# Performance work log

Hardware: AMD Instinct MI355X
Metric: run time of the kernel (lower is better)

## Reference

```python
import jax, jax.numpy as jnp
import numpy as np

L, S, M, N, E, H = 1024, 1024, 256, 8, 512, 8


def embed_rotary(x, cos, sin):
    # x: [B, T, E]; interleaved rotate-half as in RotaryPositionEncoding.embed_rotary
    x2 = jnp.stack([-x[..., 1::2], x[..., 0::2]], axis=-1).reshape(x.shape)
    return x * cos + x2 * sin


def setup_inputs() -> dict:
    key = jax.random.key(0)
    ks = jax.random.split(key, 12)
    return {
        "query": jax.random.normal(ks[0], (L, N, E), jnp.float32),
        "key": jax.random.normal(ks[1], (S, N, E), jnp.float32),
        "value": jax.random.normal(ks[2], (S, N, E), jnp.float32),
        "in_proj_weight": jax.random.normal(ks[3], (3 * E, E), jnp.float32) / np.sqrt(E).astype(np.float32),
        "in_proj_bias": jnp.zeros((3 * E,), jnp.float32),
        "out_proj_weight": jax.random.normal(ks[4], (E, E), jnp.float32) / np.sqrt(E).astype(np.float32),
        "out_proj_bias": jnp.zeros((E,), jnp.float32),
        "rot_q": jax.random.normal(ks[5], (N, L, E, 2), jnp.float32),
        "rot_k": jax.random.normal(ks[6], (N, S, E, 2), jnp.float32),
        "k_mem": jax.random.normal(ks[7], (M, N, E), jnp.float32),
        "v_mem": jax.random.normal(ks[8], (M, N, E), jnp.float32),
        "gate_attn": jax.random.normal(ks[9], (H,), jnp.float32),
        "mem_mask": jax.random.randint(ks[10], (N, M), 0, 2).astype(bool),
        "num_heads": H,
    }


def reference(query, key, value, in_proj_weight, in_proj_bias, out_proj_weight,
              out_proj_bias, rot_q, rot_k, k_mem, v_mem, gate_attn, mem_mask, num_heads):
    L_, N_, E_ = query.shape
    S_ = key.shape[0]
    H_ = num_heads
    hd = E_ // H_
    scale = float(hd) ** -0.5
    # separate q/k/v projections (qkv not identical path)
    q = query @ in_proj_weight[:E_].T + in_proj_bias[:E_]
    k = key @ in_proj_weight[E_:2 * E_].T + in_proj_bias[E_:2 * E_]
    v = value @ in_proj_weight[2 * E_:].T + in_proj_bias[2 * E_:]
    q = q * scale
    # inline rotary PE (applied in batch-first layout, then back)
    q = embed_rotary(q.transpose(1, 0, 2), rot_q[..., 0], rot_q[..., 1]).transpose(1, 0, 2)
    k = embed_rotary(k.transpose(1, 0, 2), rot_k[..., 0], rot_k[..., 1]).transpose(1, 0, 2)
    qh = q.reshape(L_, N_, H_, hd).transpose(1, 2, 0, 3)  # [N,H,L,hd]
    kh = k.reshape(S_, N_, H_, hd).transpose(1, 2, 0, 3)  # [N,H,S,hd]
    vh = v.reshape(S_, N_, H_, hd).transpose(1, 2, 0, 3)
    scores = jnp.einsum('nhld,nhsd->nhls', qh, kh)
    # slot-competition: softmax over queries (slots), then renormalize over keys
    w = jax.nn.softmax(scores, axis=2) + 1e-8
    w = w / w.sum(axis=-1, keepdims=True)
    attn = jnp.einsum('nhls,nhsd->nhld', w, vh)
    # memorizing-transformer style memory K/V branch with sigmoid head gating
    Mm = k_mem.shape[0]
    km = k_mem.reshape(Mm, N_, H_, hd).transpose(1, 2, 0, 3)  # [N,H,M,hd]
    vm = v_mem.reshape(Mm, N_, H_, hd).transpose(1, 2, 0, 3)
    sm = jnp.einsum('nhld,nhmd->nhlm', qh, km)
    sm = jnp.where(mem_mask[:, None, None, :], -1e9, sm)  # additive -inf mask
    wm = jax.nn.softmax(sm, axis=-1)
    om = jnp.einsum('nhlm,nhmd->nhld', wm, vm)
    gate = jax.nn.sigmoid(gate_attn)[None, :, None, None]  # [1,H,1,1]
    attn = gate * om + (1.0 - gate) * attn
    out = attn.transpose(2, 0, 1, 3).reshape(L_, N_, E_)  # back to [L,N,E]
    return out @ out_proj_weight.T + out_proj_bias
```

## Files before the change

### kernel.cpp

```cpp
#include <hip/hip_runtime.h>
#include <hip/hip_bf16.h>

typedef __hip_bfloat16 bf16;
typedef __bf16 bf16x8 __attribute__((ext_vector_type(8)));
typedef float f32x4 __attribute__((ext_vector_type(4)));

#define LQ 1024
#define SK 1024
#define MMEM 256
#define NB 8
#define EE 512
#define NH 8
#define HD 64
#define NBH 64

__device__ inline __bf16 tobf(float f) {
  __hip_bfloat16 h = __float2bfloat16(f);
  return *reinterpret_cast<__bf16*>(&h);
}
__device__ inline float bf2f(__bf16 x) {
  unsigned short u; __builtin_memcpy(&u, &x, 2);
  unsigned int v = (unsigned int)u << 16;
  float f; __builtin_memcpy(&f, &v, 4);
  return f;
}
__device__ inline f32x4 MFMA(bf16x8 a, bf16x8 b, f32x4 c) {
  return __builtin_amdgcn_mfma_f32_16x16x32_bf16(a, b, c, 0, 0, 0);
}

__device__ inline void gload_lds16(const bf16* g, void* l) {
  __builtin_amdgcn_global_load_lds(
      (const __attribute__((address_space(1))) void*)g,
      (__attribute__((address_space(3))) void*)l, 16, 0, 0);
}

__device__ inline bf16x8 load8(const float* p) {
  float4 a = *(const float4*)p;
  float4 b = *(const float4*)(p + 4);
  bf16x8 r;
  r[0] = tobf(a.x); r[1] = tobf(a.y); r[2] = tobf(a.z); r[3] = tobf(a.w);
  r[4] = tobf(b.x); r[5] = tobf(b.y); r[6] = tobf(b.z); r[7] = tobf(b.w);
  return r;
}

#define CVT_T0 524288
#define CVT_T3 98304
#define CVT_T4 32768
__global__ __launch_bounds__(256) void convert5(
    const float* __restrict__ q, const float* __restrict__ k,
    const float* __restrict__ v, const float* __restrict__ w,
    const float* __restrict__ o, bf16* __restrict__ qc, bf16* __restrict__ kc,
    bf16* __restrict__ vc, bf16* __restrict__ wc, bf16* __restrict__ oc)
{
  long long t = (long long)blockIdx.x * 256 + threadIdx.x;
  const float* src; bf16* dst; long long idx;
  if (t < CVT_T0)               { src = q; dst = qc; idx = t; }
  else if (t < 2 * CVT_T0)      { src = k; dst = kc; idx = t - CVT_T0; }
  else if (t < 3 * CVT_T0)      { src = v; dst = vc; idx = t - 2 * CVT_T0; }
  else if (t < 3 * CVT_T0 + CVT_T3) { src = w; dst = wc; idx = t - 3 * CVT_T0; }
  else                          { src = o; dst = oc; idx = t - 3 * CVT_T0 - CVT_T3; }
  *(bf16x8*)(dst + idx * 8) = load8(src + idx * 8);
}

__global__ __launch_bounds__(256) void gemm_proj3(
    const bf16* __restrict__ qc, const bf16* __restrict__ kc,
    const bf16* __restrict__ vc, const bf16* __restrict__ ipwb,
    const float* __restrict__ ipb, bf16* __restrict__ pq,
    bf16* __restrict__ pk, bf16* __restrict__ v_raw)
{
  __shared__ __align__(16) char smem[33792];
  __bf16* As = (__bf16*)smem;
  __bf16* Bs = (__bf16*)(smem + 16384);
  const int z = blockIdx.z;
  const bf16* A = (z == 0) ? qc : (z == 1) ? kc : vc;
  const bf16* W = ipwb + (long long)z * EE * EE;
  const float* bias = ipb + z * EE;
  const float alpha = (z == 0) ? 0.125f : 1.f;
  const int tm0 = blockIdx.y << 7, tn0 = blockIdx.x << 7;
  const int t = threadIdx.x;
  const int wave = t >> 6, lane = t & 63;
  const int wrow0 = (wave & 1) << 6, wcol0 = (wave >> 1) << 6;
  const int m16 = lane & 15, quad = lane >> 4;

  const f32x4 zero = {0.f, 0.f, 0.f, 0.f};
  f32x4 acc[4][4];
#pragma unroll
  for (int mi = 0; mi < 4; ++mi)
#pragma unroll
    for (int ni = 0; ni < 4; ++ni) acc[mi][ni] = zero;

  const bf16* Ab = A + (long long)tm0 * EE;
  const bf16* Bb = W + (long long)tn0 * EE;
  const int ob_u = wave << 10;

  for (int k0 = 0; k0 < EE; k0 += 64) {
#pragma unroll
    for (int c = 0; c < 4; ++c) {
      int ob = (c << 12) + ob_u;
      int obl = ob + (lane << 4);
      int row = obl >> 7;
      int ce = (obl & 127) >> 1;
      gload_lds16(Ab + (long long)row * EE + k0 + ce, smem + ob);
      gload_lds16(Bb + (long long)row * EE + k0 + ce, smem + 16384 + ob);
    }
    __syncthreads();
#pragma unroll
    for (int kh = 0; kh < 2; ++kh) {
      bf16x8 av[4], bv[4];
#pragma unroll
      for (int i = 0; i < 4; ++i) {
        av[i] = *(bf16x8*)(As + ((wrow0 + (i << 4) + m16) << 6) + (kh << 5) + (quad << 3));
        bv[i] = *(bf16x8*)(Bs + ((wcol0 + (i << 4) + m16) << 6) + (kh << 5) + (quad << 3));
      }
#pragma unroll
      for (int mi = 0; mi < 4; ++mi)
#pragma unroll
        for (int ni = 0; ni < 4; ++ni)
          acc[mi][ni] = MFMA(av[mi], bv[ni], acc[mi][ni]);
    }
    __syncthreads();
  }

  __bf16 (*Cs)[132] = (__bf16(*)[132])smem;
#pragma unroll
  for (int mi = 0; mi < 4; ++mi)
#pragma unroll
    for (int ni = 0; ni < 4; ++ni) {
      int col = wcol0 + (ni << 4) + m16;
      float bv = bias[tn0 + col];
#pragma unroll
      for (int r = 0; r < 4; ++r)
        Cs[wrow0 + (mi << 4) + (quad << 2) + r][col] =
            tobf((acc[mi][ni][r] + bv) * alpha);
    }
  __syncthreads();
  bf16* O = (z == 0) ? pq : (z == 1) ? pk : v_raw;
  const int crow = t >> 1, ch0 = (t & 1) << 6;
  long long gb = (long long)(tm0 + crow) * EE + tn0 + ch0;
#pragma unroll
  for (int j = 0; j < 64; j += 8)
    *(uint4*)(O + gb + j) = *(uint4*)&Cs[crow][ch0 + j];
}

__global__ __launch_bounds__(256) void rotary_kernel(
    const bf16* __restrict__ pq, const bf16* __restrict__ pk,
    const float* __restrict__ rot_q, const float* __restrict__ rot_k,
    bf16* __restrict__ Qh, bf16* __restrict__ Kh)
{
  const bf16* src = blockIdx.y ? pk : pq;
  const float* rot = blockIdx.y ? rot_k : rot_q;
  bf16* dst = blockIdx.y ? Kh : Qh;
  const int t = threadIdx.x;
  const int row = (blockIdx.x << 2) + (t >> 6);
  const int e0 = (t & 63) << 3;
  const int l = row >> 3, n = row & 7;
  bf16x8 x = *(const bf16x8*)(src + (long long)row * EE + e0);
  const float* rp = rot + ((((long long)n * LQ + l) * EE + e0) << 1);
  __bf16 vals[8];
#pragma unroll
  for (int j = 0; j < 8; j += 2) {
    float4 cs4 = *(const float4*)(rp + (j << 1));
    float x0 = bf2f(x[j]);
    float x1 = bf2f(x[j + 1]);
    vals[j]     = tobf(x0 * cs4.x - x1 * cs4.y);
    vals[j + 1] = tobf(x1 * cs4.z + x0 * cs4.w);
  }
  const int h = e0 >> 6, d0 = e0 & 63;
  *(uint4*)(dst + (((long long)(n * NH + h) * LQ + l) * HD + d0)) = *(uint4*)vals;
}

__global__ __launch_bounds__(256) void colsum_kernel(
    const bf16* __restrict__ Qh, const bf16* __restrict__ Kh,
    float* __restrict__ csum)
{
  __shared__ __align__(16) __bf16 Ks[64][72];
  __shared__ __align__(16) __bf16 Qs[64][72];
  __shared__ float cpart[64][2];
  const int b = blockIdx.y;
  const int st0 = blockIdx.x << 6;
  const int t = threadIdx.x;
  const int lrow = t >> 2, lcol = (t & 3) << 4;
  const int wave = t >> 6, lane = t & 63;
  const int wm = (wave & 1) << 5, wn = (wave >> 1) << 5;
  const int m16 = lane & 15, quad = lane >> 4;

  {
    const bf16* kp = Kh + ((long long)b * SK + st0 + lrow) * HD + lcol;
    *(bf16x8*)&Ks[lrow][lcol] = *(const bf16x8*)kp;
    *(bf16x8*)&Ks[lrow][lcol + 8] = *(const bf16x8*)(kp + 8);
  }
  __syncthreads();
  bf16x8 bk[2][2];
#pragma unroll
  for (int ni = 0; ni < 2; ++ni)
#pragma unroll
    for (int kh = 0; kh < 2; ++kh)
      bk[ni][kh] = *(bf16x8*)&Ks[wn + (ni << 4) + m16][(kh << 5) + (quad << 3)];
  __syncthreads();

  const f32x4 zero = {0.f, 0.f, 0.f, 0.f};
  float colp[2] = {0.f, 0.f};
  for (int lt = 0; lt < 16; ++lt) {
    const bf16* qp = Qh + ((long long)b * LQ + (lt << 6) + lrow) * HD + lcol;
    *(bf16x8*)&Qs[lrow][lcol] = *(const bf16x8*)qp;
    *(bf16x8*)&Qs[lrow][lcol + 8] = *(const bf16x8*)(qp + 8);
    __syncthreads();
    f32x4 s00 = zero, s01 = zero, s10 = zero, s11 = zero;
#pragma unroll
    for (int kh = 0; kh < 2; ++kh) {
      bf16x8 a0 = *(bf16x8*)&Qs[wm + m16][(kh << 5) + (quad << 3)];
      bf16x8 a1 = *(bf16x8*)&Qs[wm + 16 + m16][(kh << 5) + (quad << 3)];
      s00 = MFMA(a0, bk[0][kh], s00);
      s01 = MFMA(a0, bk[1][kh], s01);
      s10 = MFMA(a1, bk[0][kh], s10);
      s11 = MFMA(a1, bk[1][kh], s11);
    }
    f32x4 sacc[2][2] = {{s00, s01}, {s10, s11}};
#pragma unroll
    for (int mi = 0; mi < 2; ++mi)
#pragma unroll
      for (int ni = 0; ni < 2; ++ni)
#pragma unroll
        for (int r = 0; r < 4; ++r)
          colp[ni] += __expf(sacc[mi][ni][r]);
    __syncthreads();
  }
  for (int ni = 0; ni < 2; ++ni) {
    float v = colp[ni];
    v += __shfl_down(v, 32, 64);
    v += __shfl_down(v, 16, 64);
    if (quad == 0) cpart[wn + (ni << 4) + m16][wm >> 5] = v;
  }
  __syncthreads();
  if (t < 64) csum[b * SK + st0 + t] = cpart[t][0] + cpart[t][1];
}

__global__ __launch_bounds__(256) void vsum_kernel(
    const bf16* __restrict__ Vt, float* __restrict__ Vsum)
{
  int wid = blockIdx.x * 4 + (threadIdx.x >> 6);
  int lane = threadIdx.x & 63;
  const bf16* p = Vt + (long long)wid * SK + lane * 16;
  float s = 0.f;
  bf16x8 v0 = *(const bf16x8*)p;
  bf16x8 v1 = *(const bf16x8*)(p + 8);
#pragma unroll
  for (int j = 0; j < 8; ++j) s += bf2f(v0[j]) + bf2f(v1[j]);
  for (int off = 32; off; off >>= 1) s += __shfl_down(s, off, 64);
  if (lane == 0) Vsum[wid] = s;
}

__global__ __launch_bounds__(256) void attn_flash(
    const bf16* __restrict__ Qh, const bf16* __restrict__ Kh,
    const bf16* __restrict__ Vt, const float* __restrict__ csum,
    const float* __restrict__ Vsum, bf16* __restrict__ attn)
{
  __shared__ __align__(16) __bf16 Ks[64][72];
  __shared__ __align__(16) __bf16 Vs[64][72];
  __shared__ __align__(16) __bf16 Ps[64][72];
  __shared__ float rcs[SK];
  __shared__ float rpart[64][2];
  const int b = blockIdx.y;
  const int tm0 = blockIdx.x << 6;
  const int t = threadIdx.x;
  const int lrow = t >> 2, lcol = (t & 3) << 4;
  const int wave = t >> 6, lane = t & 63;
  const int wm = (wave & 1) << 5, wn = (wave >> 1) << 5;
  const int m16 = lane & 15, quad = lane >> 4;

#pragma unroll
  for (int i = 0; i < 4; ++i)
    rcs[t + i * 256] = 1.f / csum[b * SK + t + i * 256];
  {
    const bf16* qp = Qh + ((long long)b * LQ + tm0 + lrow) * HD + lcol;
    *(bf16x8*)&Ks[lrow][lcol] = *(const bf16x8*)qp;
    *(bf16x8*)&Ks[lrow][lcol + 8] = *(const bf16x8*)(qp + 8);
  }
  __syncthreads();
  bf16x8 aq[2][2];
#pragma unroll
  for (int mi = 0; mi < 2; ++mi)
#pragma unroll
    for (int kh = 0; kh < 2; ++kh)
      aq[mi][kh] = *(bf16x8*)&Ks[wm + (mi << 4) + m16][(kh << 5) + (quad << 3)];
  __syncthreads();

  const f32x4 zero = {0.f, 0.f, 0.f, 0.f};
  f32x4 o00 = zero, o01 = zero, o10 = zero, o11 = zero;
  float rsumr[2][4] = {{0.f, 0.f, 0.f, 0.f}, {0.f, 0.f, 0.f, 0.f}};

  for (int st = 0; st < 16; ++st) {
    const bf16* kp = Kh + ((long long)b * SK + (st << 6) + lrow) * HD + lcol;
    *(bf16x8*)&Ks[lrow][lcol] = *(const bf16x8*)kp;
    *(bf16x8*)&Ks[lrow][lcol + 8] = *(const bf16x8*)(kp + 8);
    const bf16* vp = Vt + ((long long)b * HD + lrow) * SK + (st << 6) + lcol;
    *(bf16x8*)&Vs[lrow][lcol] = *(const bf16x8*)vp;
    *(bf16x8*)&Vs[lrow][lcol + 8] = *(const bf16x8*)(vp + 8);
    __syncthreads();
    f32x4 s00 = zero, s01 = zero, s10 = zero, s11 = zero;
#pragma unroll
    for (int kh = 0; kh < 2; ++kh) {
      bf16x8 b0 = *(bf16x8*)&Ks[wn + m16][(kh << 5) + (quad << 3)];
      bf16x8 b1 = *(bf16x8*)&Ks[wn + 16 + m16][(kh << 5) + (quad << 3)];
      s00 = MFMA(aq[0][kh], b0, s00);
      s01 = MFMA(aq[0][kh], b1, s01);
      s10 = MFMA(aq[1][kh], b0, s10);
      s11 = MFMA(aq[1][kh], b1, s11);
    }
    f32x4 sacc[2][2] = {{s00, s01}, {s10, s11}};
#pragma unroll
    for (int mi = 0; mi < 2; ++mi)
#pragma unroll
      for (int ni = 0; ni < 2; ++ni) {
        int col = wn + (ni << 4) + m16;
        float rc = rcs[(st << 6) + col];
#pragma unroll
        for (int r = 0; r < 4; ++r) {
          float p = __expf(sacc[mi][ni][r]) * rc;
          rsumr[mi][r] += p;
          Ps[wm + (mi << 4) + (quad << 2) + r][col] = tobf(p);
        }
      }
    __syncthreads();
#pragma unroll
    for (int kh = 0; kh < 2; ++kh) {
      bf16x8 ap0 = *(bf16x8*)&Ps[wm + m16][(kh << 5) + (quad << 3)];
      bf16x8 ap1 = *(bf16x8*)&Ps[wm + 16 + m16][(kh << 5) + (quad << 3)];
      bf16x8 bv0 = *(bf16x8*)&Vs[wn + m16][(kh << 5) + (quad << 3)];
      bf16x8 bv1 = *(bf16x8*)&Vs[wn + 16 + m16][(kh << 5) + (quad << 3)];
      o00 = MFMA(ap0, bv0, o00);
      o01 = MFMA(ap0, bv1, o01);
      o10 = MFMA(ap1, bv0, o10);
      o11 = MFMA(ap1, bv1, o11);
    }
    __syncthreads();
  }
#pragma unroll
  for (int mi = 0; mi < 2; ++mi)
#pragma unroll
    for (int r = 0; r < 4; ++r) {
      float v = rsumr[mi][r];
      v += __shfl_xor(v, 1, 64);
      v += __shfl_xor(v, 2, 64);
      v += __shfl_xor(v, 4, 64);
      v += __shfl_xor(v, 8, 64);
      if (m16 == 0) rpart[wm + (mi << 4) + (quad << 2) + r][wn >> 5] = v;
    }
  __syncthreads();
  const float* vs = Vsum + b * HD;
  f32x4 oacc[2][2] = {{o00, o01}, {o10, o11}};
  for (int mi = 0; mi < 2; ++mi)
    for (int ni = 0; ni < 2; ++ni) {
      int col = wn + (ni << 4) + m16;
      float vsc = 1e-8f * vs[col];
      for (int r = 0; r < 4; ++r) {
        int row = wm + (mi << 4) + (quad << 2) + r;
        float rs = rpart[row][0] + rpart[row][1];
        Ps[row][col] = tobf((oacc[mi][ni][r] + vsc) / (rs + (float)SK * 1e-8f));
      }
    }
  __syncthreads();
  uint4 u0 = *(uint4*)&Ps[lrow][lcol];
  uint4 u1 = *(uint4*)&Ps[lrow][lcol + 8];
  long long gb = ((long long)b * LQ + tm0 + lrow) * HD + lcol;
  *(uint4*)(attn + gb) = u0;
  *(uint4*)(attn + gb + 8) = u1;
}

__global__ __launch_bounds__(256) void mem_flash(
    const bf16* __restrict__ Qh, const bf16* __restrict__ km,
    const bf16* __restrict__ vmt, const int* __restrict__ mask,
    bf16* __restrict__ omb)
{
  __shared__ __align__(16) __bf16 Ks[64][72];
  __shared__ __align__(16) __bf16 Vs[64][72];
  __shared__ __align__(16) __bf16 Ps[64][72];
  __shared__ float mskf[MMEM];
  __shared__ float rpart[64][2];
  const int b = blockIdx.y;
  const int n = b >> 3;
  const int tm0 = blockIdx.x << 6;
  const int t = threadIdx.x;
  const int wave = t >> 6, lane = t & 63;
  const int wm = (wave & 1) << 5, wn = (wave >> 1) << 5;
  const int m16 = lane & 15, quad = lane >> 4;
  const int lrow = t >> 2, lcol = (t & 3) << 4;

  mskf[t] = mask[n * MMEM + t] ? 0.f : 1.f;
  {
    const bf16* qp = Qh + ((long long)b * LQ + tm0 + lrow) * HD + lcol;
    *(bf16x8*)&Ks[lrow][lcol] = *(const bf16x8*)qp;
    *(bf16x8*)&Ks[lrow][lcol + 8] = *(const bf16x8*)(qp + 8);
  }
  __syncthreads();
  bf16x8 aq[2][2];
#pragma unroll
  for (int mi = 0; mi < 2; ++mi)
#pragma unroll
    for (int kh = 0; kh < 2; ++kh)
      aq[mi][kh] = *(bf16x8*)&Ks[wm + (mi << 4) + m16][(kh << 5) + (quad << 3)];
  __syncthreads();

  const f32x4 zero = {0.f, 0.f, 0.f, 0.f};
  f32x4 o00 = zero, o01 = zero, o10 = zero, o11 = zero;
  float rsumr[2][4] = {{0.f, 0.f, 0.f, 0.f}, {0.f, 0.f, 0.f, 0.f}};

  for (int mt = 0; mt < 4; ++mt) {
    const bf16* kp = km + ((long long)b * MMEM + (mt << 6) + lrow) * HD + lcol;
    *(bf16x8*)&Ks[lrow][lcol] = *(const bf16x8*)kp;
    *(bf16x8*)&Ks[lrow][lcol + 8] = *(const bf16x8*)(kp + 8);
    const bf16* vp = vmt + ((long long)b * HD + lrow) * MMEM + (mt << 6) + lcol;
    *(bf16x8*)&Vs[lrow][lcol] = *(const bf16x8*)vp;
    *(bf16x8*)&Vs[lrow][lcol + 8] = *(const bf16x8*)(vp + 8);
    __syncthreads();
    f32x4 s00 = zero, s01 = zero, s10 = zero, s11 = zero;
#pragma unroll
    for (int kh = 0; kh < 2; ++kh) {
      bf16x8 b0 = *(bf16x8*)&Ks[wn + m16][(kh << 5) + (quad << 3)];
      bf16x8 b1 = *(bf16x8*)&Ks[wn + 16 + m16][(kh << 5) + (quad << 3)];
      s00 = MFMA(aq[0][kh], b0, s00);
      s01 = MFMA(aq[0][kh], b1, s01);
      s10 = MFMA(aq[1][kh], b0, s10);
      s11 = MFMA(aq[1][kh], b1, s11);
    }
    f32x4 sacc[2][2] = {{s00, s01}, {s10, s11}};
#pragma unroll
    for (int mi = 0; mi < 2; ++mi)
#pragma unroll
      for (int ni = 0; ni < 2; ++ni) {
        int col = wn + (ni << 4) + m16;
        float mf = mskf[(mt << 6) + col];
#pragma unroll
        for (int r = 0; r < 4; ++r) {
          float p = __expf(sacc[mi][ni][r]) * mf;
          rsumr[mi][r] += p;
          Ps[wm + (mi << 4) + (quad << 2) + r][col] = tobf(p);
        }
      }
    __syncthreads();
#pragma unroll
    for (int kh = 0; kh < 2; ++kh) {
      bf16x8 ap0 = *(bf16x8*)&Ps[wm + m16][(kh << 5) + (quad << 3)];
      bf16x8 ap1 = *(bf16x8*)&Ps[wm + 16 + m16][(kh << 5) + (quad << 3)];
      bf16x8 bv0 = *(bf16x8*)&Vs[wn + m16][(kh << 5) + (quad << 3)];
      bf16x8 bv1 = *(bf16x8*)&Vs[wn + 16 + m16][(kh << 5) + (quad << 3)];
      o00 = MFMA(ap0, bv0, o00);
      o01 = MFMA(ap0, bv1, o01);
      o10 = MFMA(ap1, bv0, o10);
      o11 = MFMA(ap1, bv1, o11);
    }
    __syncthreads();
  }
#pragma unroll
  for (int mi = 0; mi < 2; ++mi)
#pragma unroll
    for (int r = 0; r < 4; ++r) {
      float v = rsumr[mi][r];
      v += __shfl_xor(v, 1, 64);
      v += __shfl_xor(v, 2, 64);
      v += __shfl_xor(v, 4, 64);
      v += __shfl_xor(v, 8, 64);
      if (m16 == 0) rpart[wm + (mi << 4) + (quad << 2) + r][wn >> 5] = v;
    }
  __syncthreads();
  f32x4 oacc[2][2] = {{o00, o01}, {o10, o11}};
  for (int mi = 0; mi < 2; ++mi)
    for (int ni = 0; ni < 2; ++ni) {
      int col = wn + (ni << 4) + m16;
      for (int r = 0; r < 4; ++r) {
        int row = wm + (mi << 4) + (quad << 2) + r;
        float rs = rpart[row][0] + rpart[row][1];
        Ps[row][col] = tobf(oacc[mi][ni][r] / rs);
      }
    }
  __syncthreads();
  uint4 u0 = *(uint4*)&Ps[lrow][lcol];
  uint4 u1 = *(uint4*)&Ps[lrow][lcol + 8];
  long long gb = ((long long)b * LQ + tm0 + lrow) * HD + lcol;
  *(uint4*)(omb + gb) = u0;
  *(uint4*)(omb + gb + 8) = u1;
}

__global__ __launch_bounds__(256) void gemm_out(
    const bf16* __restrict__ attn, const bf16* __restrict__ omb,
    const float* __restrict__ gate, const bf16* __restrict__ opwb,
    const float* __restrict__ opb, float* __restrict__ out)
{
  __shared__ __align__(16) __bf16 As[64][40];
  __shared__ __align__(16) __bf16 Bs[64][40];
  __shared__ float sg[NH];
  const int tm0 = blockIdx.y << 6, tn0 = blockIdx.x << 6;
  const int t = threadIdx.x;
  const int lrow = t >> 2, lk = (t & 3) << 3;
  const int wave = t >> 6, lane = t & 63;
  const int wm = (wave & 1) << 5, wn = (wave >> 1) << 5;
  const int m16 = lane & 15, quad = lane >> 4;

  if (t < NH) sg[t] = 1.f / (1.f + __expf(-gate[t]));
  __syncthreads();

  const f32x4 zero = {0.f, 0.f, 0.f, 0.f};
  f32x4 acc00 = zero, acc01 = zero, acc10 = zero, acc11 = zero;

  const int row = tm0 + lrow;
  const int l = row >> 3, n = row & 7;
  const bf16* bg = opwb + (long long)(tn0 + lrow) * EE + lk;
  for (int k0 = 0; k0 < EE; k0 += 32) {
    int e = k0 + lk;
    int h = e >> 6, d = e & 63;
    float g = sg[h];
    long long src = (((long long)(n * NH + h) * LQ) + l) * HD + d;
    bf16x8 a8 = *(const bf16x8*)(attn + src);
    bf16x8 o8 = *(const bf16x8*)(omb + src);
    bf16x8 ap;
#pragma unroll
    for (int j = 0; j < 8; ++j)
      ap[j] = tobf(g * bf2f(o8[j]) + (1.f - g) * bf2f(a8[j]));
    *(bf16x8*)&As[lrow][lk] = ap;
    *(bf16x8*)&Bs[lrow][lk] = *(const bf16x8*)(bg + k0);
    __syncthreads();
    bf16x8 a0 = *(bf16x8*)&As[wm + m16][quad << 3];
    bf16x8 a1 = *(bf16x8*)&As[wm + 16 + m16][quad << 3];
    bf16x8 b0 = *(bf16x8*)&Bs[wn + m16][quad << 3];
    bf16x8 b1 = *(bf16x8*)&Bs[wn + 16 + m16][quad << 3];
    acc00 = MFMA(a0, b0, acc00);
    acc01 = MFMA(a0, b1, acc01);
    acc10 = MFMA(a1, b0, acc10);
    acc11 = MFMA(a1, b1, acc11);
    __syncthreads();
  }
  f32x4 accs[2][2] = {{acc00, acc01}, {acc10, acc11}};
  for (int mi = 0; mi < 2; ++mi)
    for (int ni = 0; ni < 2; ++ni) {
      int col = tn0 + wn + (ni << 4) + m16;
      float bv = opb[col];
      long long base = (long long)(tm0 + wm + (mi << 4) + (quad << 2)) * EE + col;
      for (int r = 0; r < 4; ++r)
        out[base + (long long)r * EE] = accs[mi][ni][r] + bv;
    }
}

__global__ __launch_bounds__(256) void v_transpose(
    const bf16* __restrict__ raw, bf16* __restrict__ Vt)
{
  __shared__ __align__(16) __bf16 Ts[64][72];
  const int bh = blockIdx.y;
  const int n = bh >> 3, h = bh & 7;
  const int s0 = blockIdx.x << 6;
  const int t = threadIdx.x;
  const int i = t >> 2, c0 = (t & 3) << 4;
  const bf16* rp = raw + ((long long)(s0 + i) * NB + n) * EE + h * HD + c0;
  *(bf16x8*)&Ts[i][c0] = *(const bf16x8*)rp;
  *(bf16x8*)&Ts[i][c0 + 8] = *(const bf16x8*)(rp + 8);
  __syncthreads();
  const int d = t >> 2, j0 = (t & 3) << 4;
  __bf16 vals[16];
#pragma unroll
  for (int j = 0; j < 16; ++j) vals[j] = Ts[j0 + j][d];
  bf16* wp = Vt + ((long long)bh * HD + d) * SK + s0 + j0;
  *(uint4*)wp = *(uint4*)&vals[0];
  *(uint4*)(wp + 8) = *(uint4*)&vals[8];
}

__global__ __launch_bounds__(256) void mem_prep(
    const float* __restrict__ k_mem, const float* __restrict__ v_mem,
    bf16* __restrict__ km, bf16* __restrict__ vmt)
{
  __shared__ __align__(16) __bf16 Ts[64][72];
  const int bh = blockIdx.y;
  const int n = bh >> 3, h = bh & 7;
  const int m0 = blockIdx.x << 6;
  const int t = threadIdx.x;
  const int i = t >> 2, c0 = (t & 3) << 4;
  const float* kp = k_mem + ((long long)(m0 + i) * NB + n) * EE + h * HD + c0;
  const float* vp = v_mem + ((long long)(m0 + i) * NB + n) * EE + h * HD + c0;
  bf16x8 kv0 = load8(kp), kv1 = load8(kp + 8);
  bf16x8 vv0 = load8(vp), vv1 = load8(vp + 8);
  bf16* kw = km + ((long long)bh * MMEM + m0 + i) * HD + c0;
  *(bf16x8*)kw = kv0;
  *(bf16x8*)(kw + 8) = kv1;
  *(bf16x8*)&Ts[i][c0] = vv0;
  *(bf16x8*)&Ts[i][c0 + 8] = vv1;
  __syncthreads();
  const int d = t >> 2, j0 = (t & 3) << 4;
  __bf16 vals[16];
#pragma unroll
  for (int j = 0; j < 16; ++j) vals[j] = Ts[j0 + j][d];
  bf16* wp = vmt + ((long long)bh * HD + d) * MMEM + m0 + j0;
  *(uint4*)wp = *(uint4*)&vals[0];
  *(uint4*)(wp + 8) = *(uint4*)&vals[8];
}

extern "C" void kernel_launch(void* const* d_in, const int* in_sizes, int n_in,
                              void* d_out, int out_size, void* d_ws, size_t ws_size,
                              hipStream_t stream) {
  const float* query = (const float*)d_in[0];
  const float* key   = (const float*)d_in[1];
  const float* value = (const float*)d_in[2];
  const float* ipw   = (const float*)d_in[3];
  const float* ipb   = (const float*)d_in[4];
  const float* opw   = (const float*)d_in[5];
  const float* opb   = (const float*)d_in[6];
  const float* rot_q = (const float*)d_in[7];
  const float* rot_k = (const float*)d_in[8];
  const float* k_mem = (const float*)d_in[9];
  const float* v_mem = (const float*)d_in[10];
  const float* gate  = (const float*)d_in[11];
  const int*  mask   = (const int*)d_in[12];
  float* out = (float*)d_out;

  char* w = (char*)d_ws;
  size_t off = 0;
  auto carve = [&](size_t bytes) -> char* {
    char* p = w + off;
    off += (bytes + 255) & ~(size_t)255;
    return p;
  };
  bf16* qc    = (bf16*)carve((size_t)LQ * NB * EE * 2);
  bf16* kc    = (bf16*)carve((size_t)SK * NB * EE * 2);
  bf16* vc    = (bf16*)carve((size_t)SK * NB * EE * 2);
  bf16* ipwb  = (bf16*)carve((size_t)3 * EE * EE * 2);
  bf16* opwb  = (bf16*)carve((size_t)EE * EE * 2);
  bf16* v_raw = (bf16*)carve((size_t)SK * NB * EE * 2);
  bf16* Qh    = (bf16*)carve((size_t)NBH * LQ * HD * 2);
  bf16* Kh    = (bf16*)carve((size_t)NBH * SK * HD * 2);
  bf16* Vt    = (bf16*)carve((size_t)NBH * HD * SK * 2);
  bf16* km    = (bf16*)carve((size_t)NBH * MMEM * HD * 2);
  bf16* vmt   = (bf16*)carve((size_t)NBH * HD * MMEM * 2);
  float* csum = (float*)carve((size_t)NBH * SK * 4);
  float* Vsum = (float*)carve((size_t)NBH * HD * 4);
  bf16* attn  = (bf16*)carve((size_t)NBH * LQ * HD * 2);
  bf16* omb   = (bf16*)carve((size_t)NBH * LQ * HD * 2);
  if (off > ws_size) {
    hipMemsetAsync(d_out, 0, (size_t)out_size * 4, stream);
    return;
  }
  bf16* pq = attn;
  bf16* pk = omb;

  convert5<<<(3 * CVT_T0 + CVT_T3 + CVT_T4) / 256, 256, 0, stream>>>(
      query, key, value, ipw, opw, qc, kc, vc, ipwb, opwb);

  gemm_proj3<<<dim3(EE / 128, (LQ * NB) / 128, 3), 256, 0, stream>>>(
      qc, kc, vc, ipwb, ipb, pq, pk, v_raw);

  rotary_kernel<<<dim3((LQ * NB) / 4, 2), 256, 0, stream>>>(
      pq, pk, rot_q, rot_k, Qh, Kh);

  v_transpose<<<dim3(SK / 64, NBH), 256, 0, stream>>>(v_raw, Vt);
  vsum_kernel<<<(NBH * HD) / 4, 256, 0, stream>>>(Vt, Vsum);
  mem_prep<<<dim3(MMEM / 64, NBH), 256, 0, stream>>>(k_mem, v_mem, km, vmt);

  colsum_kernel<<<dim3(SK / 64, NBH), 256, 0, stream>>>(Qh, Kh, csum);

  attn_flash<<<dim3(LQ / 64, NBH), 256, 0, stream>>>(Qh, Kh, Vt, csum, Vsum, attn);
  mem_flash<<<dim3(LQ / 64, NBH), 256, 0, stream>>>(Qh, km, vmt, mask, omb);

  gemm_out<<<dim3(EE / 64, (LQ * NB) / 64, 1), 256, 0, stream>>>(attn, omb, gate, opwb, opb, out);
}
```

Baseline: 330.4 us.

## Remap block indices for XCD-local L2 reuse and register-prefetch next tiles

Remaps each kernel's flat block index so that blocks sharing the same batch-head or row tile land on the same XCD (MI355X dispatches blocks round-robin across 8 XCDs), aiming to improve L2 reuse of K/V/Q and weight tiles. In the colsum, flash attention and memory attention loops, the next K/V/Q tile is loaded into registers right after the barrier, so its global latency overlaps the current tile's MFMA work instead of stalling before each barrier. The remapping hard-codes grid shapes (the multipliers 8, 16 and 4 assume specific gridDim values), and prefetching adds register pressure.

```diff
diff --git a/kernel.cpp b/kernel.cpp
--- a/kernel.cpp
+++ b/kernel.cpp
@@ -76,7 +76,11 @@
   const bf16* W = ipwb + (long long)z * EE * EE;
   const float* bias = ipb + z * EE;
   const float alpha = (z == 0) ? 0.125f : 1.f;
-  const int tm0 = blockIdx.y << 7, tn0 = blockIdx.x << 7;
+  const int bid2 = blockIdx.y * gridDim.x + blockIdx.x;
+  const int xcd = bid2 & 7, sub = bid2 >> 3;
+  const int by = (xcd << 3) + (sub >> 2);
+  const int bx = sub & 3;
+  const int tm0 = by << 7, tn0 = bx << 7;
   const int t = threadIdx.x;
   const int wave = t >> 6, lane = t & 63;
   const int wrow0 = (wave & 1) << 6, wcol0 = (wave >> 1) << 6;
@@ -176,8 +180,10 @@
   __shared__ __align__(16) __bf16 Ks[64][72];
   __shared__ __align__(16) __bf16 Qs[64][72];
   __shared__ float cpart[64][2];
-  const int b = blockIdx.y;
-  const int st0 = blockIdx.x << 6;
+  const int bid = blockIdx.y * gridDim.x + blockIdx.x;
+  const int xcd = bid & 7, sub = bid >> 3;
+  const int b = (xcd << 3) + (sub >> 4);
+  const int st0 = (sub & 15) << 6;
   const int t = threadIdx.x;
   const int lrow = t >> 2, lcol = (t & 3) << 4;
   const int wave = t >> 6, lane = t & 63;
@@ -200,11 +206,18 @@
 
   const f32x4 zero = {0.f, 0.f, 0.f, 0.f};
   float colp[2] = {0.f, 0.f};
+  const bf16* qbase = Qh + ((long long)b * LQ + lrow) * HD + lcol;
+  bf16x8 qr0 = *(const bf16x8*)qbase;
+  bf16x8 qr1 = *(const bf16x8*)(qbase + 8);
   for (int lt = 0; lt < 16; ++lt) {
-    const bf16* qp = Qh + ((long long)b * LQ + (lt << 6) + lrow) * HD + lcol;
-    *(bf16x8*)&Qs[lrow][lcol] = *(const bf16x8*)qp;
-    *(bf16x8*)&Qs[lrow][lcol + 8] = *(const bf16x8*)(qp + 8);
-    __syncthreads();
+    *(bf16x8*)&Qs[lrow][lcol] = qr0;
+    *(bf16x8*)&Qs[lrow][lcol + 8] = qr1;
+    __syncthreads();
+    if (lt < 15) {
+      const bf16* qp = qbase + (long long)((lt + 1) << 6) * HD;
+      qr0 = *(const bf16x8*)qp;
+      qr1 = *(const bf16x8*)(qp + 8);
+    }
     f32x4 s00 = zero, s01 = zero, s10 = zero, s11 = zero;
 #pragma unroll
     for (int kh = 0; kh < 2; ++kh) {
@@ -260,8 +273,10 @@
   __shared__ __align__(16) __bf16 Ps[64][72];
   __shared__ float rcs[SK];
   __shared__ float rpart[64][2];
-  const int b = blockIdx.y;
-  const int tm0 = blockIdx.x << 6;
+  const int bid = blockIdx.y * gridDim.x + blockIdx.x;
+  const int xcd = bid & 7, sub = bid >> 3;
+  const int b = (xcd << 3) + (sub >> 4);
+  const int tm0 = (sub & 15) << 6;
   const int t = threadIdx.x;
   const int lrow = t >> 2, lcol = (t & 3) << 4;
   const int wave = t >> 6, lane = t & 63;
@@ -289,14 +304,27 @@
   f32x4 o00 = zero, o01 = zero, o10 = zero, o11 = zero;
   float rsumr[2][4] = {{0.f, 0.f, 0.f, 0.f}, {0.f, 0.f, 0.f, 0.f}};
 
+  const bf16* kbase = Kh + ((long long)b * SK + lrow) * HD + lcol;
+  const bf16* vbase = Vt + ((long long)b * HD + lrow) * SK + lcol;
+  bf16x8 kr0 = *(const bf16x8*)kbase;
+  bf16x8 kr1 = *(const bf16x8*)(kbase + 8);
+  bf16x8 vr0 = *(const bf16x8*)vbase;
+  bf16x8 vr1 = *(const bf16x8*)(vbase + 8);
+
   for (int st = 0; st < 16; ++st) {
-    const bf16* kp = Kh + ((long long)b * SK + (st << 6) + lrow) * HD + lcol;
-    *(bf16x8*)&Ks[lrow][lcol] = *(const bf16x8*)kp;
-    *(bf16x8*)&Ks[lrow][lcol + 8] = *(const bf16x8*)(kp + 8);
-    const bf16* vp = Vt + ((long long)b * HD + lrow) * SK + (st << 6) + lcol;
-    *(bf16x8*)&Vs[lrow][lcol] = *(const bf16x8*)vp;
-    *(bf16x8*)&Vs[lrow][lcol + 8] = *(const bf16x8*)(vp + 8);
-    __syncthreads();
+    *(bf16x8*)&Ks[lrow][lcol] = kr0;
+    *(bf16x8*)&Ks[lrow][lcol + 8] = kr1;
+    *(bf16x8*)&Vs[lrow][lcol] = vr0;
+    *(bf16x8*)&Vs[lrow][lcol + 8] = vr1;
+    __syncthreads();
+    if (st < 15) {
+      const bf16* kp = kbase + (long long)((st + 1) << 6) * HD;
+      const bf16* vp = vbase + ((st + 1) << 6);
+      kr0 = *(const bf16x8*)kp;
+      kr1 = *(const bf16x8*)(kp + 8);
+      vr0 = *(const bf16x8*)vp;
+      vr1 = *(const bf16x8*)(vp + 8);
+    }
     f32x4 s00 = zero, s01 = zero, s10 = zero, s11 = zero;
 #pragma unroll
     for (int kh = 0; kh < 2; ++kh) {
@@ -377,9 +405,11 @@
   __shared__ __align__(16) __bf16 Ps[64][72];
   __shared__ float mskf[MMEM];
   __shared__ float rpart[64][2];
-  const int b = blockIdx.y;
+  const int bid = blockIdx.y * gridDim.x + blockIdx.x;
+  const int xcd = bid & 7, sub = bid >> 3;
+  const int b = (xcd << 3) + (sub >> 4);
+  const int tm0 = (sub & 15) << 6;
   const int n = b >> 3;
-  const int tm0 = blockIdx.x << 6;
   const int t = threadIdx.x;
   const int wave = t >> 6, lane = t & 63;
   const int wm = (wave & 1) << 5, wn = (wave >> 1) << 5;
@@ -405,14 +435,27 @@
   f32x4 o00 = zero, o01 = zero, o10 = zero, o11 = zero;
   float rsumr[2][4] = {{0.f, 0.f, 0.f, 0.f}, {0.f, 0.f, 0.f, 0.f}};
 
+  const bf16* kbase = km + ((long long)b * MMEM + lrow) * HD + lcol;
+  const bf16* vbase = vmt + ((long long)b * HD + lrow) * MMEM + lcol;
+  bf16x8 kr0 = *(const bf16x8*)kbase;
+  bf16x8 kr1 = *(const bf16x8*)(kbase + 8);
+  bf16x8 vr0 = *(const bf16x8*)vbase;
+  bf16x8 vr1 = *(const bf16x8*)(vbase + 8);
+
   for (int mt = 0; mt < 4; ++mt) {
-    const bf16* kp = km + ((long long)b * MMEM + (mt << 6) + lrow) * HD + lcol;
-    *(bf16x8*)&Ks[lrow][lcol] = *(const bf16x8*)kp;
-    *(bf16x8*)&Ks[lrow][lcol + 8] = *(const bf16x8*)(kp + 8);
-    const bf16* vp = vmt + ((long long)b * HD + lrow) * MMEM + (mt << 6) + lcol;
-    *(bf16x8*)&Vs[lrow][lcol] = *(const bf16x8*)vp;
-    *(bf16x8*)&Vs[lrow][lcol + 8] = *(const bf16x8*)(vp + 8);
-    __syncthreads();
+    *(bf16x8*)&Ks[lrow][lcol] = kr0;
+    *(bf16x8*)&Ks[lrow][lcol + 8] = kr1;
+    *(bf16x8*)&Vs[lrow][lcol] = vr0;
+    *(bf16x8*)&Vs[lrow][lcol + 8] = vr1;
+    __syncthreads();
+    if (mt < 3) {
+      const bf16* kp = kbase + (long long)((mt + 1) << 6) * HD;
+      const bf16* vp = vbase + ((mt + 1) << 6);
+      kr0 = *(const bf16x8*)kp;
+      kr1 = *(const bf16x8*)(kp + 8);
+      vr0 = *(const bf16x8*)vp;
+      vr1 = *(const bf16x8*)(vp + 8);
+    }
     f32x4 s00 = zero, s01 = zero, s10 = zero, s11 = zero;
 #pragma unroll
     for (int kh = 0; kh < 2; ++kh) {
@@ -489,7 +532,11 @@
   __shared__ __align__(16) __bf16 As[64][40];
   __shared__ __align__(16) __bf16 Bs[64][40];
   __shared__ float sg[NH];
-  const int tm0 = blockIdx.y << 6, tn0 = blockIdx.x << 6;
+  const int bid = blockIdx.y * gridDim.x + blockIdx.x;
+  const int xcd = bid & 7, sub = bid >> 3;
+  const int by = (xcd << 4) + (sub >> 3);
+  const int bx = sub & 7;
+  const int tm0 = by << 6, tn0 = bx << 6;
   const int t = threadIdx.x;
   const int lrow = t >> 2, lk = (t & 3) << 3;
   const int wave = t >> 6, lane = t & 63;
```

After: 309.9 us. -6.2%, faster.
